# Optimization experiments

Measured on AMD Instinct MI355X. Metric: run time of the kernel, lower is better.

The kernel has to match this reference:

```python
import jax, jax.numpy as jnp
import numpy as np

DIM = 1024
HEADS = 16
HEAD_DIM = DIM // HEADS
HIDDEN = 4 * DIM
SCALE = HEAD_DIM ** -0.5
EPS = 1e-5


def _layernorm(x, g, b):
    mu = jnp.mean(x, axis=-1, keepdims=True)
    var = jnp.mean(jnp.square(x - mu), axis=-1, keepdims=True)
    return (x - mu) * jax.lax.rsqrt(var + EPS) * g + b


def setup_inputs() -> dict:
    key = jax.random.key(0)
    ks = jax.random.split(key, 8)
    B, N, C = 4, 2048, DIM
    s = 0.02
    return {
        "x": jax.random.normal(ks[0], (B, N, C), dtype=jnp.float32),
        "ln1_g": jnp.ones((C,), jnp.float32),
        "ln1_b": jnp.zeros((C,), jnp.float32),
        "qkv_w": jax.random.normal(ks[1], (3 * C, C), jnp.float32) * s,
        "proj_w": jax.random.normal(ks[2], (C, C), jnp.float32) * s,
        "proj_b": jnp.zeros((C,), jnp.float32),
        "ln2_g": jnp.ones((C,), jnp.float32),
        "ln2_b": jnp.zeros((C,), jnp.float32),
        "fc1_w": jax.random.normal(ks[3], (HIDDEN, C), jnp.float32) * s,
        "fc1_b": jnp.zeros((HIDDEN,), jnp.float32),
        "fc2_w": jax.random.normal(ks[4], (C, HIDDEN), jnp.float32) * s,
        "fc2_b": jnp.zeros((C,), jnp.float32),
    }


def reference(x, ln1_g, ln1_b, qkv_w, proj_w, proj_b, ln2_g, ln2_b, fc1_w, fc1_b, fc2_w, fc2_b):
    B, N, C = x.shape
    # --- attention branch ---
    h = _layernorm(x, ln1_g, ln1_b)
    qkv = h @ qkv_w.T                                  # [B,N,3C]
    qkv = qkv.reshape(B, N, 3, HEADS, HEAD_DIM)
    q = qkv[:, :, 0].transpose(0, 2, 1, 3) * SCALE      # [B,H,N,D]
    k = qkv[:, :, 1].transpose(0, 2, 1, 3)
    v = qkv[:, :, 2].transpose(0, 2, 1, 3)
    attn = jax.nn.softmax(jnp.einsum('bhqd,bhkd->bhqk', q, k), axis=-1)
    o = jnp.einsum('bhqk,bhkd->bhqd', attn, v)          # [B,H,N,D]
    o = o.transpose(0, 2, 1, 3).reshape(B, N, C)
    x = x + (o @ proj_w.T + proj_b)
    # --- MLP branch ---
    h2 = _layernorm(x, ln2_g, ln2_b)
    h2 = jax.nn.gelu(h2 @ fc1_w.T + fc1_b, approximate=False)
    x = x + (h2 @ fc2_w.T + fc2_b)
    return x
```

## Files before the change

kernel.cpp:

```cpp
#include <hip/hip_runtime.h>
#include <math.h>

typedef __bf16 bf16;
typedef __attribute__((ext_vector_type(8))) __bf16 bf16x8;
typedef __attribute__((ext_vector_type(4))) __bf16 bf16x4;
typedef __attribute__((ext_vector_type(4))) float floatx4;

#define MFMA(a, b, c) __builtin_amdgcn_mfma_f32_16x16x32_bf16((a), (b), (c), 0, 0, 0)

__device__ __forceinline__ void async_load16(const bf16* g, bf16* l) {
    __builtin_amdgcn_global_load_lds((const __attribute__((address_space(1))) void*)(g),
                                     (__attribute__((address_space(3))) void*)(l), 16, 0, 0);
}

__device__ __forceinline__ float gelu_fast(float t) {
    const float g  = 0.7978845608f * (t + 0.044715f * t * t * t);
    const float u  = __builtin_amdgcn_exp2f(g * 2.885390082f);
    const float th = (u - 1.0f) * __builtin_amdgcn_rcpf(u + 1.0f);
    return 0.5f * t * (1.0f + th);
}

__global__ __launch_bounds__(256) void cast4_kernel(const float* __restrict__ a0,
                                                    const float* __restrict__ a1,
                                                    const float* __restrict__ a2,
                                                    const float* __restrict__ a3,
                                                    bf16* __restrict__ o0,
                                                    bf16* __restrict__ o1,
                                                    bf16* __restrict__ o2,
                                                    bf16* __restrict__ o3) {
    long i = (long)blockIdx.x * 256 + threadIdx.x;
    const float* in;
    bf16* out;
    long off;
    if (i < 393216) { in = a0; out = o0; off = i; }
    else if (i < 524288) { in = a1; out = o1; off = i - 393216; }
    else if (i < 1048576) { in = a2; out = o2; off = i - 524288; }
    else { in = a3; out = o3; off = i - 1048576; }
    const float4 a = ((const float4*)in)[2 * off];
    const float4 b = ((const float4*)in)[2 * off + 1];
    bf16x8 o;
    o[0] = (bf16)a.x; o[1] = (bf16)a.y; o[2] = (bf16)a.z; o[3] = (bf16)a.w;
    o[4] = (bf16)b.x; o[5] = (bf16)b.y; o[6] = (bf16)b.z; o[7] = (bf16)b.w;
    *(bf16x8*)(out + off * 8) = o;
}

__global__ __launch_bounds__(256) void ln_kernel(const float* __restrict__ x,
                                                 const float* __restrict__ g,
                                                 const float* __restrict__ b,
                                                 bf16* __restrict__ out) {
    const int row = blockIdx.x;
    const int tid = threadIdx.x;
    const float4 v = ((const float4*)(x + (long)row * 1024))[tid];
    float s  = v.x + v.y + v.z + v.w;
    float s2 = v.x * v.x + v.y * v.y + v.z * v.z + v.w * v.w;
#pragma unroll
    for (int off = 32; off > 0; off >>= 1) {
        s  += __shfl_xor(s, off, 64);
        s2 += __shfl_xor(s2, off, 64);
    }
    __shared__ float red[8];
    const int wave = tid >> 6, lane = tid & 63;
    if (lane == 0) { red[wave] = s; red[wave + 4] = s2; }
    __syncthreads();
    const float ts  = red[0] + red[1] + red[2] + red[3];
    const float ts2 = red[4] + red[5] + red[6] + red[7];
    const float mu   = ts * (1.0f / 1024.0f);
    const float rstd = rsqrtf(ts2 * (1.0f / 1024.0f) - mu * mu + 1e-5f);
    const float4 gg = ((const float4*)g)[tid];
    const float4 bb = ((const float4*)b)[tid];
    bf16x4 o;
    o[0] = (bf16)((v.x - mu) * rstd * gg.x + bb.x);
    o[1] = (bf16)((v.y - mu) * rstd * gg.y + bb.y);
    o[2] = (bf16)((v.z - mu) * rstd * gg.z + bb.z);
    o[3] = (bf16)((v.w - mu) * rstd * gg.w + bb.w);
    *(bf16x4*)(out + (long)row * 1024 + tid * 4) = o;
}

template <int EPI>
__global__ __launch_bounds__(256, 4)
void gemm_bt(const bf16* __restrict__ A, const bf16* __restrict__ B,
             const float* __restrict__ bias, const float* __restrict__ resid,
             void* __restrict__ Cout, bf16* __restrict__ vtout, int M, int N, int K) {
    __shared__ __align__(16) bf16 sA[128 * 64];
    __shared__ __align__(16) bf16 sB[128 * 64];
    const int tid  = threadIdx.x;
    const int lane = tid & 63;
    const int wave = tid >> 6;
    const int wm = (wave >> 1) << 6;
    const int wn = (wave & 1) << 6;
    const int c15 = lane & 15;
    const int kq  = lane >> 4;
    const int c7  = lane & 7;
    const long tileM = (long)blockIdx.y * 128;
    const long tileN = (long)blockIdx.x * 128;

    floatx4 acc[4][4] = {};

    const int srow = tid >> 3;
    const int scol = ((tid & 7) ^ (srow & 7)) * 8;
    const bf16* Abase = A + (tileM + srow) * (long)K + scol;
    const bf16* Bbase = B + (tileN + srow) * (long)K + scol;
    bf16* sAw = sA + tid * 8;
    bf16* sBw = sB + tid * 8;

    for (int k0 = 0; k0 < K; k0 += 64) {
        __syncthreads();
#pragma unroll
        for (int it = 0; it < 4; ++it) {
            async_load16(Abase + (long)it * 32 * K + k0, sAw + it * 2048);
            async_load16(Bbase + (long)it * 32 * K + k0, sBw + it * 2048);
        }
        __syncthreads();
#pragma unroll
        for (int kk = 0; kk < 2; ++kk) {
            bf16x8 a[4], b[4];
#pragma unroll
            for (int i = 0; i < 4; ++i) {
                const int ch = ((kk << 2) + kq) ^ c7;
                a[i] = *(const bf16x8*)(sA + (wm + i * 16 + c15) * 64 + ch * 8);
                b[i] = *(const bf16x8*)(sB + (wn + i * 16 + c15) * 64 + ch * 8);
            }
#pragma unroll
            for (int i = 0; i < 4; ++i)
#pragma unroll
                for (int j = 0; j < 4; ++j)
                    acc[i][j] = MFMA(a[i], b[j], acc[i][j]);
        }
    }

#pragma unroll
    for (int i = 0; i < 4; ++i)
#pragma unroll
        for (int j = 0; j < 4; ++j) {
            if (EPI == 3 && tileN >= 2048) {
                const long gnv  = tileN - 2048 + wn + j * 16 + c15;
                const long tokb = tileM + wm + i * 16 + kq * 4;
                const long row  = ((tokb >> 11) << 10) + gnv;
                bf16x4 ov;
#pragma unroll
                for (int r = 0; r < 4; ++r) ov[r] = (bf16)acc[i][j][r];
                *(bf16x4*)(vtout + row * 2048 + (tokb & 2047)) = ov;
            } else {
#pragma unroll
                for (int r = 0; r < 4; ++r) {
                    const long gm = tileM + wm + i * 16 + kq * 4 + r;
                    const long gn = tileN + wn + j * 16 + c15;
                    const float v = acc[i][j][r];
                    if (EPI == 0 || EPI == 3) {
                        ((bf16*)Cout)[gm * N + gn] = (bf16)v;
                    } else if (EPI == 1) {
                        ((float*)Cout)[gm * N + gn] = v + bias[gn] + resid[gm * N + gn];
                    } else {
                        ((bf16*)Cout)[gm * N + gn] = (bf16)gelu_fast(v + bias[gn]);
                    }
                }
            }
        }
}

__global__ __launch_bounds__(256, 4)
void attn_kernel(const bf16* __restrict__ qkv, const bf16* __restrict__ vt,
                 bf16* __restrict__ o) {
    __shared__ __align__(16) bf16 sK[64 * 64];
    __shared__ __align__(16) bf16 sV[64 * 64];
    __shared__ __align__(16) bf16 sP[8][16 * 72];
    const int bh = blockIdx.x, b = bh >> 4, h = bh & 15;
    const int q0 = blockIdx.y * 128;
    const int tid = threadIdx.x, lane = tid & 63, wave = tid >> 6;
    const int c15 = lane & 15, kq = lane >> 4, c7 = lane & 7;

    bf16x8 qf[2][2];
#pragma unroll
    for (int t = 0; t < 2; ++t) {
        const bf16* qrow =
            qkv + ((long)(b * 2048 + q0 + wave * 32 + t * 16 + c15)) * 3072 + h * 64;
#pragma unroll
        for (int kk = 0; kk < 2; ++kk) {
            const bf16x8 raw = *(const bf16x8*)(qrow + kk * 32 + kq * 8);
            bf16x8 sc;
#pragma unroll
            for (int e = 0; e < 8; ++e) sc[e] = (bf16)((float)raw[e] * 0.18033688f);
            qf[t][kk] = sc;
        }
    }

    floatx4 oacc[2][4] = {};
    float l_s[2] = {0.f, 0.f};

    const bf16* kbase = qkv + ((long)b * 2048) * 3072 + 1024 + h * 64;
    const bf16* vbase = vt + (long)bh * 64 * 2048;

    const int srow = tid >> 3;
    const int scol = ((tid & 7) ^ (srow & 7)) * 8;
    bf16* sKw = sK + tid * 8;
    bf16* sVw = sV + tid * 8;
    bf16* sP0 = sP[wave * 2];
    bf16* sP1 = sP[wave * 2 + 1];

    for (int kv0 = 0; kv0 < 2048; kv0 += 64) {
        __syncthreads();
#pragma unroll
        for (int it = 0; it < 2; ++it) {
            async_load16(kbase + (long)(kv0 + it * 32 + srow) * 3072 + scol, sKw + it * 2048);
            async_load16(vbase + (long)(it * 32 + srow) * 2048 + kv0 + scol, sVw + it * 2048);
        }
        __syncthreads();

        floatx4 s0[4], s1[4];
#pragma unroll
        for (int j = 0; j < 4; ++j) {
            const bf16x8 k0 = *(const bf16x8*)(sK + (j * 16 + c15) * 64 + ((kq ^ c7) * 8));
            const bf16x8 k1 = *(const bf16x8*)(sK + (j * 16 + c15) * 64 + (((4 | kq) ^ c7) * 8));
            floatx4 a0 = {0.f, 0.f, 0.f, 0.f}, a1 = {0.f, 0.f, 0.f, 0.f};
            a0 = MFMA(k0, qf[0][0], a0);
            a0 = MFMA(k1, qf[0][1], a0);
            a1 = MFMA(k0, qf[1][0], a1);
            a1 = MFMA(k1, qf[1][1], a1);
            s0[j] = a0;
            s1[j] = a1;
        }

#pragma unroll
        for (int t = 0; t < 2; ++t) {
            floatx4* s = (t == 0) ? s0 : s1;
            bf16* sPt = (t == 0) ? sP0 : sP1;
            float rs = 0.f;
#pragma unroll
            for (int j = 0; j < 4; ++j) {
                const float p0 = __builtin_amdgcn_exp2f(s[j][0]);
                const float p1 = __builtin_amdgcn_exp2f(s[j][1]);
                const float p2 = __builtin_amdgcn_exp2f(s[j][2]);
                const float p3 = __builtin_amdgcn_exp2f(s[j][3]);
                rs += (p0 + p1) + (p2 + p3);
                bf16x4 pk;
                pk[0] = (bf16)p0; pk[1] = (bf16)p1; pk[2] = (bf16)p2; pk[3] = (bf16)p3;
                *(bf16x4*)(sPt + c15 * 72 + j * 16 + kq * 4) = pk;
            }
            l_s[t] += rs;
        }

        bf16x8 pf[2][2];
#pragma unroll
        for (int t = 0; t < 2; ++t) {
            bf16* sPt = (t == 0) ? sP0 : sP1;
            pf[t][0] = *(const bf16x8*)(sPt + c15 * 72 + kq * 8);
            pf[t][1] = *(const bf16x8*)(sPt + c15 * 72 + 32 + kq * 8);
        }
#pragma unroll
        for (int i = 0; i < 4; ++i) {
            const bf16x8 v0 = *(const bf16x8*)(sV + (i * 16 + c15) * 64 + ((kq ^ c7) * 8));
            const bf16x8 v1 = *(const bf16x8*)(sV + (i * 16 + c15) * 64 + (((4 | kq) ^ c7) * 8));
            oacc[0][i] = MFMA(v0, pf[0][0], oacc[0][i]);
            oacc[0][i] = MFMA(v1, pf[0][1], oacc[0][i]);
            oacc[1][i] = MFMA(v0, pf[1][0], oacc[1][i]);
            oacc[1][i] = MFMA(v1, pf[1][1], oacc[1][i]);
        }
    }

#pragma unroll
    for (int t = 0; t < 2; ++t) {
        float rs = l_s[t];
        rs += __shfl_xor(rs, 16, 64);
        rs += __shfl_xor(rs, 32, 64);
        const float linv = 1.0f / rs;
        const long tok = (long)(b * 2048 + q0 + wave * 32 + t * 16 + c15);
#pragma unroll
        for (int i = 0; i < 4; ++i) {
            bf16x4 ov;
#pragma unroll
            for (int r = 0; r < 4; ++r) ov[r] = (bf16)(oacc[t][i][r] * linv);
            *(bf16x4*)(o + tok * 1024 + h * 64 + i * 16 + kq * 4) = ov;
        }
    }
}

extern "C" void kernel_launch(void* const* d_in, const int* in_sizes, int n_in,
                              void* d_out, int out_size, void* d_ws, size_t ws_size,
                              hipStream_t stream) {
    const float* x      = (const float*)d_in[0];
    const float* ln1_g  = (const float*)d_in[1];
    const float* ln1_b  = (const float*)d_in[2];
    const float* qkv_w  = (const float*)d_in[3];
    const float* proj_w = (const float*)d_in[4];
    const float* proj_b = (const float*)d_in[5];
    const float* ln2_g  = (const float*)d_in[6];
    const float* ln2_b  = (const float*)d_in[7];
    const float* fc1_w  = (const float*)d_in[8];
    const float* fc1_b  = (const float*)d_in[9];
    const float* fc2_w  = (const float*)d_in[10];
    const float* fc2_b  = (const float*)d_in[11];
    float* out = (float*)d_out;

    char* ws = (char*)d_ws;
    bf16* actbuf = (bf16*)(ws);
    bf16* wqkv   = (bf16*)(ws + (16ull << 20));
    bf16* wproj  = (bf16*)(ws + (22ull << 20));
    bf16* wfc1   = (bf16*)(ws + (24ull << 20));
    bf16* wfc2   = (bf16*)(ws + (32ull << 20));
    bf16* qkvbuf = (bf16*)(ws + (40ull << 20));
    bf16* vtbuf  = (bf16*)(ws + (88ull << 20));
    bf16* gbuf   = (bf16*)(ws + (40ull << 20));

    const dim3 blk(256);

    cast4_kernel<<<6144, blk, 0, stream>>>(qkv_w, proj_w, fc1_w, fc2_w,
                                           wqkv, wproj, wfc1, wfc2);

    ln_kernel<<<8192, blk, 0, stream>>>(x, ln1_g, ln1_b, actbuf);

    gemm_bt<3><<<dim3(24, 64), blk, 0, stream>>>(actbuf, wqkv, nullptr, nullptr,
                                                 qkvbuf, vtbuf, 8192, 3072, 1024);
    attn_kernel<<<dim3(64, 16), blk, 0, stream>>>(qkvbuf, vtbuf, actbuf);

    gemm_bt<1><<<dim3(8, 64), blk, 0, stream>>>(actbuf, wproj, proj_b, x,
                                                d_out, nullptr, 8192, 1024, 1024);

    ln_kernel<<<8192, blk, 0, stream>>>(out, ln2_g, ln2_b, actbuf);

    gemm_bt<2><<<dim3(32, 64), blk, 0, stream>>>(actbuf, wfc1, fc1_b, nullptr,
                                                 gbuf, nullptr, 8192, 4096, 1024);
    gemm_bt<1><<<dim3(8, 64), blk, 0, stream>>>(gbuf, wfc2, fc2_b, out,
                                                d_out, nullptr, 8192, 1024, 4096);
}
```

Measured before the change: 494.7 us.

## Add 256x256-tile 512-thread GEMM with staged async loads for QKV and FC1

Adds a new GEMM kernel using 256x256 output tiles with 8 waves per block. Global-to-LDS async loads are split into four quarter stages interleaved with MFMA phases, with setprio around the compute. QKV and FC1 projections now use it, which raises data reuse per LDS byte and overlaps loads with math. The old gemm_bt epilogue is simplified, dropping the V-transpose path, since only the new kernel handles EPI 3. The bigger tile gives fewer blocks (384 and 512), which may hurt wave balance, and register pressure rises with 32 accumulators per thread.

```diff
diff --git a/kernel.cpp b/kernel.cpp
--- a/kernel.cpp
+++ b/kernel.cpp
@@ -132,6 +132,158 @@
     for (int i = 0; i < 4; ++i)
 #pragma unroll
         for (int j = 0; j < 4; ++j) {
+#pragma unroll
+            for (int r = 0; r < 4; ++r) {
+                const long gm = tileM + wm + i * 16 + kq * 4 + r;
+                const long gn = tileN + wn + j * 16 + c15;
+                const float v = acc[i][j][r];
+                if (EPI == 0) {
+                    ((bf16*)Cout)[gm * N + gn] = (bf16)v;
+                } else if (EPI == 1) {
+                    ((float*)Cout)[gm * N + gn] = v + bias[gn] + resid[gm * N + gn];
+                } else {
+                    ((bf16*)Cout)[gm * N + gn] = (bf16)gelu_fast(v + bias[gn]);
+                }
+            }
+        }
+}
+
+template <int EPI>
+__global__ __launch_bounds__(512, 2)
+void gemm_bt256(const bf16* __restrict__ A, const bf16* __restrict__ B,
+                const float* __restrict__ bias, const float* __restrict__ resid,
+                void* __restrict__ Cout, bf16* __restrict__ vtout,
+                int M, int N, int K) {
+    __shared__ __align__(16) bf16 s[4][2][8192];
+    const int tid  = threadIdx.x;
+    const int lane = tid & 63;
+    const int wave = tid >> 6;
+    const int c15 = lane & 15;
+    const int kq  = lane >> 4;
+    const int c7  = lane & 7;
+    const int hA   = wave >> 2;
+    const int hB   = (wave >> 1) & 1;
+    const int wsub = (wave & 1) << 6;
+    const int wm = hA << 7;
+    const int wn = (hB << 7) | wsub;
+    const long tileM = (long)blockIdx.y * 256;
+    const long tileN = (long)blockIdx.x * 256;
+    const int nk = K >> 6;
+
+    floatx4 acc[8][4] = {};
+
+    const int srow = tid >> 3;
+    const int scol = ((tid & 7) ^ (srow & 7)) << 3;
+    const bf16* ga0 = A + (tileM + srow) * (long)K + scol;
+    const bf16* ga1 = ga0 + 128 * (long)K;
+    const bf16* gb0 = B + (tileN + srow) * (long)K + scol;
+    const bf16* gb1 = gb0 + 128 * (long)K;
+
+#define STAGE(H, GP, kt)                                          \
+    do {                                                          \
+        if ((kt) < nk) {                                          \
+            const bf16* _g = (GP) + ((long)(kt) << 6);            \
+            bf16* _d = &s[H][(kt) & 1][tid * 8];                  \
+            async_load16(_g, _d);                                 \
+            async_load16(_g + 64 * (long)K, _d + 4096);           \
+        }                                                         \
+    } while (0)
+
+    STAGE(2, gb0, 0); STAGE(3, gb1, 0);
+    STAGE(0, ga0, 0); STAGE(1, ga1, 0);
+    STAGE(2, gb0, 1); STAGE(3, gb1, 1);
+    asm volatile("s_waitcnt vmcnt(4)" ::: "memory");
+    __builtin_amdgcn_s_barrier();
+
+    bf16x8 af[4][2], bL[2][2], bH[2][2];
+
+#define RD(P, r, ks) \
+    (*(const bf16x8*)((P) + ((r) << 6) + (((((ks) << 2) | kq) ^ c7) << 3)))
+
+    for (int t = 0; t < nk; ++t) {
+        const bf16* pa = s[hA][t & 1];
+        const bf16* pb = s[2 + hB][t & 1];
+
+#pragma unroll
+        for (int i = 0; i < 4; ++i) {
+            af[i][0] = RD(pa, i * 16 + c15, 0);
+            af[i][1] = RD(pa, i * 16 + c15, 1);
+        }
+#pragma unroll
+        for (int j = 0; j < 2; ++j) {
+            bL[j][0] = RD(pb, wsub + j * 16 + c15, 0);
+            bL[j][1] = RD(pb, wsub + j * 16 + c15, 1);
+        }
+        STAGE(0, ga0, t + 1);
+        __builtin_amdgcn_s_barrier();
+        __builtin_amdgcn_s_setprio(1);
+#pragma unroll
+        for (int i = 0; i < 4; ++i)
+#pragma unroll
+            for (int j = 0; j < 2; ++j) {
+                acc[i][j] = MFMA(af[i][0], bL[j][0], acc[i][j]);
+                acc[i][j] = MFMA(af[i][1], bL[j][1], acc[i][j]);
+            }
+        __builtin_amdgcn_s_setprio(0);
+        __builtin_amdgcn_s_barrier();
+
+#pragma unroll
+        for (int j = 0; j < 2; ++j) {
+            bH[j][0] = RD(pb, wsub + 32 + j * 16 + c15, 0);
+            bH[j][1] = RD(pb, wsub + 32 + j * 16 + c15, 1);
+        }
+        STAGE(1, ga1, t + 1);
+        __builtin_amdgcn_s_barrier();
+        __builtin_amdgcn_s_setprio(1);
+#pragma unroll
+        for (int i = 0; i < 4; ++i)
+#pragma unroll
+            for (int j = 0; j < 2; ++j) {
+                acc[i][2 + j] = MFMA(af[i][0], bH[j][0], acc[i][2 + j]);
+                acc[i][2 + j] = MFMA(af[i][1], bH[j][1], acc[i][2 + j]);
+            }
+        __builtin_amdgcn_s_setprio(0);
+        __builtin_amdgcn_s_barrier();
+
+#pragma unroll
+        for (int i = 0; i < 4; ++i) {
+            af[i][0] = RD(pa, 64 + i * 16 + c15, 0);
+            af[i][1] = RD(pa, 64 + i * 16 + c15, 1);
+        }
+        STAGE(2, gb0, t + 2);
+        __builtin_amdgcn_s_barrier();
+        __builtin_amdgcn_s_setprio(1);
+#pragma unroll
+        for (int i = 0; i < 4; ++i)
+#pragma unroll
+            for (int j = 0; j < 2; ++j) {
+                acc[4 + i][2 + j] = MFMA(af[i][0], bH[j][0], acc[4 + i][2 + j]);
+                acc[4 + i][2 + j] = MFMA(af[i][1], bH[j][1], acc[4 + i][2 + j]);
+            }
+        __builtin_amdgcn_s_setprio(0);
+        __builtin_amdgcn_s_barrier();
+
+        STAGE(3, gb1, t + 2);
+        __builtin_amdgcn_s_barrier();
+        __builtin_amdgcn_s_setprio(1);
+#pragma unroll
+        for (int i = 0; i < 4; ++i)
+#pragma unroll
+            for (int j = 0; j < 2; ++j) {
+                acc[4 + i][j] = MFMA(af[i][0], bL[j][0], acc[4 + i][j]);
+                acc[4 + i][j] = MFMA(af[i][1], bL[j][1], acc[4 + i][j]);
+            }
+        __builtin_amdgcn_s_setprio(0);
+        asm volatile("s_waitcnt vmcnt(4)" ::: "memory");
+        __builtin_amdgcn_s_barrier();
+    }
+#undef STAGE
+#undef RD
+
+#pragma unroll
+    for (int i = 0; i < 8; ++i)
+#pragma unroll
+        for (int j = 0; j < 4; ++j) {
             if (EPI == 3 && tileN >= 2048) {
                 const long gnv  = tileN - 2048 + wn + j * 16 + c15;
                 const long tokb = tileM + wm + i * 16 + kq * 4;
@@ -302,14 +454,15 @@
     bf16* gbuf   = (bf16*)(ws + (40ull << 20));
 
     const dim3 blk(256);
+    const dim3 blk512(512);
 
     cast4_kernel<<<6144, blk, 0, stream>>>(qkv_w, proj_w, fc1_w, fc2_w,
                                            wqkv, wproj, wfc1, wfc2);
 
     ln_kernel<<<8192, blk, 0, stream>>>(x, ln1_g, ln1_b, actbuf);
 
-    gemm_bt<3><<<dim3(24, 64), blk, 0, stream>>>(actbuf, wqkv, nullptr, nullptr,
-                                                 qkvbuf, vtbuf, 8192, 3072, 1024);
+    gemm_bt256<3><<<dim3(12, 32), blk512, 0, stream>>>(actbuf, wqkv, nullptr, nullptr,
+                                                       qkvbuf, vtbuf, 8192, 3072, 1024);
     attn_kernel<<<dim3(64, 16), blk, 0, stream>>>(qkvbuf, vtbuf, actbuf);
 
     gemm_bt<1><<<dim3(8, 64), blk, 0, stream>>>(actbuf, wproj, proj_b, x,
@@ -317,8 +470,8 @@
 
     ln_kernel<<<8192, blk, 0, stream>>>(out, ln2_g, ln2_b, actbuf);
 
-    gemm_bt<2><<<dim3(32, 64), blk, 0, stream>>>(actbuf, wfc1, fc1_b, nullptr,
-                                                 gbuf, nullptr, 8192, 4096, 1024);
+    gemm_bt256<2><<<dim3(16, 32), blk512, 0, stream>>>(actbuf, wfc1, fc1_b, nullptr,
+                                                       gbuf, nullptr, 8192, 4096, 1024);
     gemm_bt<1><<<dim3(8, 64), blk, 0, stream>>>(gbuf, wfc2, fc2_b, out,
                                                 d_out, nullptr, 8192, 1024, 4096);
 }
```

Result: no change. 491.2 us (-0.7%).
